# Kernel tuning notes

Hardware: AMD Instinct MI355X
Metric: run time of the kernel (lower is better)

The kernel has to match this reference:

```python
import jax, jax.numpy as jnp
import numpy as np
import math

B, S, HID = 1, 2048, 1024
NH, NKV = 16, 4
HD = HID // NH          # 64
GROUPS = NH // NKV      # 4
ROPE_BASE = 10000.0


def setup_inputs() -> dict:
    key = jax.random.key(0)
    ks = jax.random.split(key, 5)
    hidden_states = jax.random.normal(ks[0], (B, S, HID), dtype=jnp.float32)
    # additive causal mask: 0 on/below diagonal, -1e9 above
    causal = jnp.triu(jnp.full((S, S), -1e9, dtype=jnp.float32), k=1)
    attention_mask = causal[None, None, :, :]
    position_ids = jnp.arange(S, dtype=jnp.int32)[None, :]
    sc = 0.02
    Wq = jax.random.normal(ks[1], (NH * HD, HID), dtype=jnp.float32) * sc
    Wk = jax.random.normal(ks[2], (NKV * HD, HID), dtype=jnp.float32) * sc
    Wv = jax.random.normal(ks[3], (NKV * HD, HID), dtype=jnp.float32) * sc
    Wo = jax.random.normal(ks[4], (HID, NH * HD), dtype=jnp.float32) * sc
    return {"hidden_states": hidden_states, "attention_mask": attention_mask,
            "position_ids": position_ids, "Wq": Wq, "Wk": Wk, "Wv": Wv, "Wo": Wo}


def _rotate_half(x):
    x1, x2 = jnp.split(x, 2, axis=-1)
    return jnp.concatenate([-x2, x1], axis=-1)


def _rope_cos_sin(position_ids, dtype):
    # LlamaRotaryEmbedding: inv_freq over even dims, emb = [freqs, freqs]
    inv_freq = 1.0 / (ROPE_BASE ** (jnp.arange(0, HD, 2, dtype=jnp.float32) / HD))
    freqs = position_ids.astype(jnp.float32)[..., None] * inv_freq  # [B,S,HD/2]
    emb = jnp.concatenate([freqs, freqs], axis=-1)                  # [B,S,HD]
    return jnp.cos(emb).astype(dtype)[:, None], jnp.sin(emb).astype(dtype)[:, None]


def reference(hidden_states, attention_mask, position_ids, Wq, Wk, Wv, Wo):
    b, q_len, _ = hidden_states.shape
    # torch Linear: y = x @ W.T  (W is [out, in])
    q = jnp.einsum('bsh,oh->bso', hidden_states, Wq).reshape(b, q_len, NH, HD).transpose(0, 2, 1, 3)
    k = jnp.einsum('bsh,oh->bso', hidden_states, Wk).reshape(b, q_len, NKV, HD).transpose(0, 2, 1, 3)
    v = jnp.einsum('bsh,oh->bso', hidden_states, Wv).reshape(b, q_len, NKV, HD).transpose(0, 2, 1, 3)

    cos, sin = _rope_cos_sin(position_ids, q.dtype)  # [B,1,S,HD]
    q = q * cos + _rotate_half(q) * sin
    k = k * cos + _rotate_half(k) * sin

    # repeat_kv (GQA expansion)
    k = jnp.repeat(k, GROUPS, axis=1)  # [B,NH,S,HD]
    v = jnp.repeat(v, GROUPS, axis=1)

    scores = jnp.einsum('bhqd,bhkd->bhqk', q, k) / math.sqrt(HD)
    scores = scores + attention_mask
    attn = jax.nn.softmax(scores.astype(jnp.float32), axis=-1).astype(q.dtype)
    out = jnp.einsum('bhqk,bhkd->bhqd', attn, v)
    out = out.transpose(0, 2, 1, 3).reshape(b, q_len, NH * HD)
    return jnp.einsum('bso,ho->bsh', out, Wo)
```

## Files before the change

kernel.cpp:

```cpp
#include <hip/hip_runtime.h>
#include <hip/hip_bf16.h>
#include <math.h>

#define S_LEN 2048
#define HIDN  1024
#define K_DIM 1024
#define NHEAD 16
#define NKVH  4
#define HD    64

typedef __bf16 bf16x8 __attribute__((ext_vector_type(8)));
typedef float  f32x4  __attribute__((ext_vector_type(4)));

static __device__ __forceinline__ unsigned short f2bf(float f) {
  union { float f; unsigned u; } v; v.f = f;
  unsigned u = v.u;
  u += 0x7fffu + ((u >> 16) & 1u);
  return (unsigned short)(u >> 16);
}

static __device__ __forceinline__ void gload_lds16(const unsigned short* g, unsigned short* l) {
  __builtin_amdgcn_global_load_lds((const __attribute__((address_space(1))) void*)g,
                                   (__attribute__((address_space(3))) void*)l, 16, 0, 0);
}

__global__ __launch_bounds__(256) void prep_kernel(const float* __restrict__ hs,
                                                   const float* __restrict__ Wq,
                                                   const float* __restrict__ Wk,
                                                   const float* __restrict__ Wv,
                                                   const float* __restrict__ Wo,
                                                   const int* __restrict__ pos,
                                                   unsigned short* __restrict__ hsb,
                                                   unsigned short* __restrict__ Wqkv,
                                                   unsigned short* __restrict__ Wob,
                                                   float2* __restrict__ cstab) {
  const int gid = blockIdx.x * 256 + threadIdx.x;
  if (gid < 1179648) {
    const float* src; unsigned short* dst; int i;
    if (gid < 524288)       { src = hs; dst = hsb;            i = gid; }
    else if (gid < 786432)  { src = Wq; dst = Wqkv;           i = gid - 524288; }
    else if (gid < 851968)  { src = Wk; dst = Wqkv + 1048576; i = gid - 786432; }
    else if (gid < 917504)  { src = Wv; dst = Wqkv + 1310720; i = gid - 851968; }
    else                    { src = Wo; dst = Wob;            i = gid - 917504; }
    float4 v = *(const float4*)(src + (size_t)i * 4);
    ushort4 u;
    u.x = f2bf(v.x); u.y = f2bf(v.y); u.z = f2bf(v.z); u.w = f2bf(v.w);
    *(ushort4*)(dst + (size_t)i * 4) = u;
  } else {
    int e = gid - 1179648;
    int s = e >> 5, ir = e & 31;
    float p = (float)pos[s];
    float ang = p * __expf(-(float)ir * 0.28782314f);
    float c, sn;
    sincosf(ang, &sn, &c);
    cstab[e] = make_float2(c, sn);
  }
}

template <bool ROPE>
__global__ __launch_bounds__(256) void gemm_kernel(const unsigned short* __restrict__ A,
                                                   const unsigned short* __restrict__ B,
                                                   float* __restrict__ C,
                                                   const float2* __restrict__ cstab,
                                                   unsigned short* __restrict__ Qr,
                                                   unsigned short* __restrict__ Kr,
                                                   unsigned short* __restrict__ Vtmp) {
  __shared__ unsigned short As[2][64][64];
  __shared__ unsigned short Bs[2][128][64];
  const int m0 = blockIdx.x * 64, n0 = blockIdx.y * 128;
  const int t = threadIdx.x, w = t >> 6, lane = t & 63;
  const int lr = lane & 15, lg = lane >> 4;
  const int m_off = (w & 1) * 32, n_off = (w >> 1) * 64;
  const int rsub = lane >> 3;
  const int cole = ((lane & 7) * 8) ^ (rsub << 3);
  f32x4 acc[2][4] = {};

#define GSTAGE(b, kt) do {                                                     \
    _Pragma("unroll")                                                          \
    for (int c = 0; c < 2; ++c) {                                              \
      int ch = w * 2 + c;                                                      \
      gload_lds16(A + (size_t)(m0 + ch * 8 + rsub) * K_DIM + (kt) * 64 + cole, \
                  &As[b][0][0] + ch * 512);                                    \
    }                                                                          \
    _Pragma("unroll")                                                          \
    for (int c = 0; c < 4; ++c) {                                              \
      int ch = w * 4 + c;                                                      \
      gload_lds16(B + (size_t)(n0 + ch * 8 + rsub) * K_DIM + (kt) * 64 + cole, \
                  &Bs[b][0][0] + ch * 512);                                    \
    }                                                                          \
  } while (0)

  int cur = 0;
  GSTAGE(0, 0);
  for (int kt = 0; kt < 16; ++kt) {
    __syncthreads();
    if (kt + 1 < 16) GSTAGE(cur ^ 1, kt + 1);
#pragma unroll
    for (int kc = 0; kc < 2; ++kc) {
      bf16x8 af[2], bfg[4];
#pragma unroll
      for (int i = 0; i < 2; ++i) {
        int row = m_off + i * 16 + lr;
        af[i] = *(const bf16x8*)((const char*)&As[cur][0][0] + row * 128 +
                                 ((kc * 64 + lg * 16) ^ ((lr & 7) << 4)));
      }
#pragma unroll
      for (int j = 0; j < 4; ++j) {
        int row = n_off + j * 16 + lr;
        bfg[j] = *(const bf16x8*)((const char*)&Bs[cur][0][0] + row * 128 +
                                  ((kc * 64 + lg * 16) ^ ((lr & 7) << 4)));
      }
#pragma unroll
      for (int i = 0; i < 2; ++i)
#pragma unroll
        for (int j = 0; j < 4; ++j)
          acc[i][j] = __builtin_amdgcn_mfma_f32_16x16x32_bf16(af[i], bfg[j], acc[i][j], 0, 0, 0);
    }
    cur ^= 1;
  }

  if constexpr (ROPE) {
    const int col64 = n0 + n_off;
    const int hh = col64 >> 6;
#pragma unroll
    for (int i = 0; i < 2; ++i) {
#pragma unroll
      for (int r = 0; r < 4; ++r) {
        int srow = m0 + m_off + i * 16 + lg * 4 + r;
        if (hh < 20) {
          unsigned short* dst = (hh < 16) ? (Qr + ((size_t)hh * S_LEN + srow) * HD)
                                          : (Kr + ((size_t)(hh - 16) * S_LEN + srow) * HD);
          float sc = (hh < 16) ? 0.125f : 1.0f;
#pragma unroll
          for (int j = 0; j < 2; ++j) {
            int d0 = j * 16 + lr;
            float2 cs = cstab[(size_t)srow * 32 + d0];
            float v0 = acc[i][j][r] * sc, v1 = acc[i][j + 2][r] * sc;
            dst[d0]      = f2bf(v0 * cs.x - v1 * cs.y);
            dst[d0 + 32] = f2bf(v1 * cs.x + v0 * cs.y);
          }
        } else {
          int vcol = col64 - 1280;
#pragma unroll
          for (int j = 0; j < 4; ++j)
            Vtmp[(size_t)srow * 256 + vcol + j * 16 + lr] = f2bf(acc[i][j][r]);
        }
      }
    }
  } else {
#pragma unroll
    for (int i = 0; i < 2; ++i)
#pragma unroll
      for (int j = 0; j < 4; ++j)
#pragma unroll
        for (int r = 0; r < 4; ++r)
          C[(size_t)(m0 + m_off + i * 16 + lg * 4 + r) * 1024 + n0 + n_off + j * 16 + lr] =
              acc[i][j][r];
  }
}

__global__ __launch_bounds__(256) void transpose_v(const unsigned short* __restrict__ Vtmp,
                                                   unsigned short* __restrict__ Vt) {
  __shared__ unsigned short tile[64][72];
  const int kh = blockIdx.x & 3, st = blockIdx.x >> 2;
  const int s0 = st * 64;
  const int t = threadIdx.x;
  const int r = t >> 3, c = (t & 7) * 8;
#pragma unroll
  for (int p = 0; p < 2; ++p) {
    int row = r + p * 32;
    uint4 v = *(const uint4*)(Vtmp + (size_t)(s0 + row) * 256 + kh * 64 + c);
    *(uint4*)&tile[row][c] = v;
  }
  __syncthreads();
#pragma unroll
  for (int p = 0; p < 2; ++p) {
    int d = r + p * 32;
    int sc = (t & 7) * 8;
    union { unsigned short s[8]; uint4 q; } u;
#pragma unroll
    for (int e = 0; e < 8; ++e) u.s[e] = tile[sc + e][d];
    *(uint4*)(Vt + ((size_t)kh * HD + d) * S_LEN + s0 + sc) = u.q;
  }
}

__global__ __launch_bounds__(256) void attn_kernel(const unsigned short* __restrict__ Qr,
                                                   const unsigned short* __restrict__ Kr,
                                                   const unsigned short* __restrict__ Vt,
                                                   unsigned short* __restrict__ Ob) {
  __shared__ unsigned short Ks[2][64][64];
  __shared__ unsigned short Vs[2][64][64];
  const int h = blockIdx.x & 15;
  const int qt = 31 - (blockIdx.x >> 4);
  const int kh = h >> 2;
  const int q0 = qt * 64;
  const int t = threadIdx.x, w = t >> 6, lane = t & 63;
  const int lr = lane & 15, lg = lane >> 4;
  const int qabs = q0 + w * 16 + lr;
  const int src0 = ((lane >> 4) & 1) * 32 + lr;
  const int src1 = src0 + 16;
  const bool hi2 = (lg & 2);

  const unsigned short* qb = Qr + ((size_t)h * S_LEN + qabs) * HD + lg * 8;
  bf16x8 qf0 = *(const bf16x8*)qb;
  bf16x8 qf1 = *(const bf16x8*)(qb + 32);

  float m_run = -1e30f, l_run = 0.f;
  f32x4 oacc[4] = {};

  const int rsub = lane >> 3;
  const int cole = ((lane & 7) * 8) ^ (rsub << 3);

#define ASTAGE(b, kt) do {                                                        \
    int k0s = (kt) * 64;                                                          \
    _Pragma("unroll")                                                             \
    for (int c = 0; c < 4; ++c) {                                                 \
      int ch = w * 4 + c;                                                         \
      int rowc = (ch & 7) * 8 + rsub;                                             \
      if (ch < 8)                                                                 \
        gload_lds16(Kr + ((size_t)kh * S_LEN + k0s + rowc) * HD + cole,           \
                    &Ks[b][0][0] + (ch & 7) * 512);                               \
      else                                                                        \
        gload_lds16(Vt + ((size_t)kh * HD + rowc) * S_LEN + k0s + cole,           \
                    &Vs[b][0][0] + (ch & 7) * 512);                               \
    }                                                                             \
  } while (0)

  int cur = 0;
  const int nkt = qt + 1;
  ASTAGE(0, 0);
  for (int kt = 0; kt < nkt; ++kt) {
    __syncthreads();
    if (kt + 1 < nkt) ASTAGE(cur ^ 1, kt + 1);
    const int k0 = kt * 64;

    f32x4 sacc[4] = {};
#pragma unroll
    for (int kc = 0; kc < 2; ++kc) {
      bf16x8 qq = kc ? qf1 : qf0;
#pragma unroll
      for (int nt = 0; nt < 4; ++nt) {
        int row = nt * 16 + lr;
        bf16x8 kf = *(const bf16x8*)((const char*)&Ks[cur][0][0] + row * 128 +
                                     ((kc * 64 + lg * 16) ^ ((lr & 7) << 4)));
        sacc[nt] = __builtin_amdgcn_mfma_f32_16x16x32_bf16(kf, qq, sacc[nt], 0, 0, 0);
      }
    }

    float p[16];
#pragma unroll
    for (int nt = 0; nt < 4; ++nt)
#pragma unroll
      for (int r = 0; r < 4; ++r) p[nt * 4 + r] = sacc[nt][r];

    if (kt == qt) {
      int lim = qabs - k0 - lg * 4;
#pragma unroll
      for (int nt = 0; nt < 4; ++nt)
#pragma unroll
        for (int r = 0; r < 4; ++r)
          if (nt * 16 + r > lim) p[nt * 4 + r] = -1e30f;
    }

    float t0 = fmaxf(fmaxf(p[0], p[1]), fmaxf(p[2], p[3]));
    float t1 = fmaxf(fmaxf(p[4], p[5]), fmaxf(p[6], p[7]));
    float t2 = fmaxf(fmaxf(p[8], p[9]), fmaxf(p[10], p[11]));
    float t3 = fmaxf(fmaxf(p[12], p[13]), fmaxf(p[14], p[15]));
    float tmax = fmaxf(fmaxf(t0, t1), fmaxf(t2, t3));
    tmax = fmaxf(tmax, __shfl_xor(tmax, 16));
    tmax = fmaxf(tmax, __shfl_xor(tmax, 32));

    if (__any(tmax > m_run + 8.0f)) {
      float mnew = fmaxf(m_run, tmax);
      float f = __expf(m_run - mnew);
      l_run *= f;
#pragma unroll
      for (int dt = 0; dt < 4; ++dt) oacc[dt] *= f;
      m_run = mnew;
    }

    float lsum = 0.f;
#pragma unroll
    for (int e = 0; e < 16; ++e) {
      p[e] = __expf(p[e] - m_run);
      lsum += p[e];
    }
    lsum += __shfl_xor(lsum, 16);
    lsum += __shfl_xor(lsum, 32);
    l_run += lsum;

    unsigned pk[4][2];
#pragma unroll
    for (int nt = 0; nt < 4; ++nt)
#pragma unroll
      for (int rr = 0; rr < 2; ++rr) {
        union { __hip_bfloat162 b; unsigned u; } cv;
        cv.b = __float22bfloat162_rn(make_float2(p[nt * 4 + 2 * rr], p[nt * 4 + 2 * rr + 1]));
        pk[nt][rr] = cv.u;
      }

#pragma unroll
    for (int kcp = 0; kcp < 2; ++kcp) {
      const int nta = kcp * 2, ntb = kcp * 2 + 1;
      unsigned a0 = __shfl(pk[nta][0], src0), b0 = __shfl(pk[ntb][0], src0);
      unsigned a1 = __shfl(pk[nta][1], src0), b1 = __shfl(pk[ntb][1], src0);
      unsigned a2 = __shfl(pk[nta][0], src1), b2 = __shfl(pk[ntb][0], src1);
      unsigned a3 = __shfl(pk[nta][1], src1), b3 = __shfl(pk[ntb][1], src1);
      union { bf16x8 v; unsigned u[4]; } pf;
      pf.u[0] = hi2 ? b0 : a0;
      pf.u[1] = hi2 ? b1 : a1;
      pf.u[2] = hi2 ? b2 : a2;
      pf.u[3] = hi2 ? b3 : a3;
#pragma unroll
      for (int dt = 0; dt < 4; ++dt) {
        int row = dt * 16 + lr;
        bf16x8 vf = *(const bf16x8*)((const char*)&Vs[cur][0][0] + row * 128 +
                                     ((kcp * 64 + lg * 16) ^ ((lr & 7) << 4)));
        oacc[dt] = __builtin_amdgcn_mfma_f32_16x16x32_bf16(vf, pf.v, oacc[dt], 0, 0, 0);
      }
    }
    cur ^= 1;
  }

  float inv = 1.f / l_run;
#pragma unroll
  for (int dt = 0; dt < 4; ++dt) {
    ushort4 u;
    u.x = f2bf(oacc[dt][0] * inv);
    u.y = f2bf(oacc[dt][1] * inv);
    u.z = f2bf(oacc[dt][2] * inv);
    u.w = f2bf(oacc[dt][3] * inv);
    *(ushort4*)(Ob + (size_t)qabs * HIDN + h * HD + dt * 16 + lg * 4) = u;
  }
}

extern "C" void kernel_launch(void* const* d_in, const int* in_sizes, int n_in,
                              void* d_out, int out_size, void* d_ws, size_t ws_size,
                              hipStream_t stream) {
  const float* hs = (const float*)d_in[0];
  const int* pos = (const int*)d_in[2];
  const float* Wq = (const float*)d_in[3];
  const float* Wk = (const float*)d_in[4];
  const float* Wv = (const float*)d_in[5];
  const float* Wo = (const float*)d_in[6];
  float* out = (float*)d_out;

  char* ws = (char*)d_ws;
  unsigned short* hsb  = (unsigned short*)(ws);
  unsigned short* Wqkv = (unsigned short*)(ws + 4194304);
  unsigned short* Wob  = (unsigned short*)(ws + 7340032);
  float2*         cstab = (float2*)(ws + 9437184);
  unsigned short* Qr   = (unsigned short*)(ws + 10485760);
  unsigned short* Kr   = (unsigned short*)(ws + 14680064);
  unsigned short* Vtmp = (unsigned short*)(ws + 15728640);
  unsigned short* Vt   = (unsigned short*)(ws + 16777216);
  unsigned short* Ob   = (unsigned short*)(ws + 17825792);

  dim3 blk(256);
  prep_kernel<<<4864, blk, 0, stream>>>(hs, Wq, Wk, Wv, Wo, pos, hsb, Wqkv, Wob, cstab);
  gemm_kernel<true><<<dim3(32, 12), blk, 0, stream>>>(hsb, Wqkv, nullptr, cstab, Qr, Kr, Vtmp);
  transpose_v<<<128, blk, 0, stream>>>(Vtmp, Vt);
  attn_kernel<<<512, blk, 0, stream>>>(Qr, Kr, Vt, Ob);
  gemm_kernel<false><<<dim3(32, 8), blk, 0, stream>>>(Ob, Wob, out, nullptr, nullptr, nullptr, nullptr);
}
```

Measured before the change: 89.13 us.

## Split causal attention along the key dimension with a separate merge kernel

Replaces the single attention kernel with a split-KV scheme. Each query tile's key range is cut into chunks of up to 8 key tiles, which gives 1280 balanced blocks instead of 512 blocks of very uneven causal length. Each block writes fp32 partial outputs and its (max, sum) stats to workspace. A new merge kernel then rescales and combines the partials and writes the bf16 output. The cost is an extra launch and roughly 30+ MB of extra fp32 partial-output traffic.

After: 90.68 us. About the same (+1.7%).

```diff
diff --git a/kernel.cpp b/kernel.cpp
--- a/kernel.cpp
+++ b/kernel.cpp
@@ -184,16 +184,26 @@
   }
 }
 
-__global__ __launch_bounds__(256) void attn_kernel(const unsigned short* __restrict__ Qr,
-                                                   const unsigned short* __restrict__ Kr,
-                                                   const unsigned short* __restrict__ Vt,
-                                                   unsigned short* __restrict__ Ob) {
+__global__ __launch_bounds__(256) void attn_part(const unsigned short* __restrict__ Qr,
+                                                 const unsigned short* __restrict__ Kr,
+                                                 const unsigned short* __restrict__ Vt,
+                                                 float* __restrict__ Opart,
+                                                 float* __restrict__ Mlpart) {
   __shared__ unsigned short Ks[2][64][64];
   __shared__ unsigned short Vs[2][64][64];
-  const int h = blockIdx.x & 15;
-  const int qt = 31 - (blockIdx.x >> 4);
+  const int bid = blockIdx.x;
+  const int h = bid / 80;
+  const int remr = 79 - (bid - h * 80);
+  int qt, ck;
+  if (remr < 8)       { qt = remr;                 ck = 0; }
+  else if (remr < 24) { int e = remr - 8;  qt = 8  + (e >> 1); ck = e & 1; }
+  else if (remr < 48) { int e = remr - 24; int d3 = e / 3; qt = 16 + d3; ck = e - d3 * 3; }
+  else                { int e = remr - 48; qt = 24 + (e >> 2); ck = e & 3; }
   const int kh = h >> 2;
   const int q0 = qt * 64;
+  const int kt0 = ck * 8;
+  const int kt1 = (kt0 + 8 < qt + 1) ? kt0 + 8 : qt + 1;
+
   const int t = threadIdx.x, w = t >> 6, lane = t & 63;
   const int lr = lane & 15, lg = lane >> 4;
   const int qabs = q0 + w * 16 + lr;
@@ -227,11 +237,10 @@
   } while (0)
 
   int cur = 0;
-  const int nkt = qt + 1;
-  ASTAGE(0, 0);
-  for (int kt = 0; kt < nkt; ++kt) {
+  ASTAGE(0, kt0);
+  for (int kt = kt0; kt < kt1; ++kt) {
     __syncthreads();
-    if (kt + 1 < nkt) ASTAGE(cur ^ 1, kt + 1);
+    if (kt + 1 < kt1) ASTAGE(cur ^ 1, kt + 1);
     const int k0 = kt * 64;
 
     f32x4 sacc[4] = {};
@@ -322,15 +331,54 @@
     cur ^= 1;
   }
 
-  float inv = 1.f / l_run;
+  const int slot = (h * 32 + qt) * 4 + ck;
+  float* ob = Opart + (size_t)slot * 4096;
+#pragma unroll
+  for (int dt = 0; dt < 4; ++dt)
+    *(f32x4*)(ob + (((w * 4 + dt) * 4 + lg) * 16 + lr) * 4) = oacc[dt];
+  if (lg == 0)
+    *(float2*)(Mlpart + ((size_t)slot * 64 + w * 16 + lr) * 2) = make_float2(m_run, l_run);
+}
+
+__global__ __launch_bounds__(256) void attn_merge(const float* __restrict__ Opart,
+                                                  const float* __restrict__ Mlpart,
+                                                  unsigned short* __restrict__ Ob) {
+  const int h = blockIdx.x >> 5, qt = blockIdx.x & 31;
+  const int nch = (qt >> 3) + 1;
+  const int slotb = (h * 32 + qt) * 4;
+  const int t = threadIdx.x, w = t >> 6, lane = t & 63;
+  const int lr = lane & 15, lg = lane >> 4;
+  const int q = w * 16 + lr;
+
+  float mc[4], lc[4];
+  float mstar = -1e30f;
+  for (int c = 0; c < nch; ++c) {
+    float2 ml = *(const float2*)(Mlpart + ((size_t)(slotb + c) * 64 + q) * 2);
+    mc[c] = ml.x; lc[c] = ml.y;
+    mstar = fmaxf(mstar, ml.x);
+  }
+  float wgt[4];
+  float lsum = 0.f;
+  for (int c = 0; c < nch; ++c) {
+    wgt[c] = __expf(mc[c] - mstar);
+    lsum += wgt[c] * lc[c];
+  }
+  const float inv = 1.f / lsum;
+
 #pragma unroll
   for (int dt = 0; dt < 4; ++dt) {
+    f32x4 a = {};
+    for (int c = 0; c < nch; ++c) {
+      f32x4 v = *(const f32x4*)(Opart + (size_t)(slotb + c) * 4096 +
+                                (((w * 4 + dt) * 4 + lg) * 16 + lr) * 4);
+      a += v * wgt[c];
+    }
     ushort4 u;
-    u.x = f2bf(oacc[dt][0] * inv);
-    u.y = f2bf(oacc[dt][1] * inv);
-    u.z = f2bf(oacc[dt][2] * inv);
-    u.w = f2bf(oacc[dt][3] * inv);
-    *(ushort4*)(Ob + (size_t)qabs * HIDN + h * HD + dt * 16 + lg * 4) = u;
+    u.x = f2bf(a[0] * inv);
+    u.y = f2bf(a[1] * inv);
+    u.z = f2bf(a[2] * inv);
+    u.w = f2bf(a[3] * inv);
+    *(ushort4*)(Ob + (size_t)(qt * 64 + q) * HIDN + h * HD + dt * 16 + lg * 4) = u;
   }
 }
 
@@ -346,20 +394,23 @@
   float* out = (float*)d_out;
 
   char* ws = (char*)d_ws;
-  unsigned short* hsb  = (unsigned short*)(ws);
-  unsigned short* Wqkv = (unsigned short*)(ws + 4194304);
-  unsigned short* Wob  = (unsigned short*)(ws + 7340032);
+  unsigned short* hsb   = (unsigned short*)(ws);
+  unsigned short* Wqkv  = (unsigned short*)(ws + 4194304);
+  unsigned short* Wob   = (unsigned short*)(ws + 7340032);
   float2*         cstab = (float2*)(ws + 9437184);
-  unsigned short* Qr   = (unsigned short*)(ws + 10485760);
-  unsigned short* Kr   = (unsigned short*)(ws + 14680064);
-  unsigned short* Vtmp = (unsigned short*)(ws + 15728640);
-  unsigned short* Vt   = (unsigned short*)(ws + 16777216);
-  unsigned short* Ob   = (unsigned short*)(ws + 17825792);
+  unsigned short* Qr    = (unsigned short*)(ws + 10485760);
+  unsigned short* Kr    = (unsigned short*)(ws + 14680064);
+  unsigned short* Vtmp  = (unsigned short*)(ws + 15728640);
+  unsigned short* Vt    = (unsigned short*)(ws + 16777216);
+  unsigned short* Ob    = (unsigned short*)(ws + 17825792);
+  float*          Opart = (float*)(ws + 22020096);
+  float*          Mlpart= (float*)(ws + 55574528);
 
   dim3 blk(256);
   prep_kernel<<<4864, blk, 0, stream>>>(hs, Wq, Wk, Wv, Wo, pos, hsb, Wqkv, Wob, cstab);
   gemm_kernel<true><<<dim3(32, 12), blk, 0, stream>>>(hsb, Wqkv, nullptr, cstab, Qr, Kr, Vtmp);
   transpose_v<<<128, blk, 0, stream>>>(Vtmp, Vt);
-  attn_kernel<<<512, blk, 0, stream>>>(Qr, Kr, Vt, Ob);
+  attn_part<<<1280, blk, 0, stream>>>(Qr, Kr, Vt, Opart, Mlpart);
+  attn_merge<<<512, blk, 0, stream>>>(Opart, Mlpart, Ob);
   gemm_kernel<false><<<dim3(32, 8), blk, 0, stream>>>(Ob, Wob, out, nullptr, nullptr, nullptr, nullptr);
 }
```

## Replace LDS-staged attention block with single-wave blocks reading K/V directly

Applied to the files above, without the earlier changes.

Attention now runs as 2048 one-wave blocks, each handling a 16-query strip, instead of 512 four-wave blocks per 64-query tile. The LDS double-buffering and __syncthreads are removed, and K and V fragments are loaded straight from global memory (through cache), with V prefetched into registers before the softmax. s_setprio is added around the MFMA sections. This finer split aims to improve load balance across the causal triangle and remove sync overhead, at the cost of losing K/V reuse across the four waves that previously shared each LDS tile, which raises global/L2 traffic.

Measured after the change: 119.6 us. 34.2% more time.

```diff
diff --git a/kernel.cpp b/kernel.cpp
--- a/kernel.cpp
+++ b/kernel.cpp
@@ -184,19 +184,18 @@
   }
 }
 
-__global__ __launch_bounds__(256) void attn_kernel(const unsigned short* __restrict__ Qr,
-                                                   const unsigned short* __restrict__ Kr,
-                                                   const unsigned short* __restrict__ Vt,
-                                                   unsigned short* __restrict__ Ob) {
-  __shared__ unsigned short Ks[2][64][64];
-  __shared__ unsigned short Vs[2][64][64];
-  const int h = blockIdx.x & 15;
-  const int qt = 31 - (blockIdx.x >> 4);
+__global__ __launch_bounds__(64) void attn_wave(const unsigned short* __restrict__ Qr,
+                                                const unsigned short* __restrict__ Kr,
+                                                const unsigned short* __restrict__ Vt,
+                                                unsigned short* __restrict__ Ob) {
+  const int bid = blockIdx.x;
+  const int h = bid & 15;
+  const int strip = 127 - (bid >> 4);
   const int kh = h >> 2;
-  const int q0 = qt * 64;
-  const int t = threadIdx.x, w = t >> 6, lane = t & 63;
+  const int q0 = strip * 16;
+  const int lane = threadIdx.x;
   const int lr = lane & 15, lg = lane >> 4;
-  const int qabs = q0 + w * 16 + lr;
+  const int qabs = q0 + lr;
   const int src0 = ((lane >> 4) & 1) * 32 + lr;
   const int src1 = src0 + 16;
   const bool hi2 = (lg & 2);
@@ -205,47 +204,35 @@
   bf16x8 qf0 = *(const bf16x8*)qb;
   bf16x8 qf1 = *(const bf16x8*)(qb + 32);
 
+  const unsigned short* Kh = Kr + (size_t)kh * S_LEN * HD;
+  const unsigned short* Vh = Vt + (size_t)kh * HD * S_LEN;
+
   float m_run = -1e30f, l_run = 0.f;
   f32x4 oacc[4] = {};
-
-  const int rsub = lane >> 3;
-  const int cole = ((lane & 7) * 8) ^ (rsub << 3);
-
-#define ASTAGE(b, kt) do {                                                        \
-    int k0s = (kt) * 64;                                                          \
-    _Pragma("unroll")                                                             \
-    for (int c = 0; c < 4; ++c) {                                                 \
-      int ch = w * 4 + c;                                                         \
-      int rowc = (ch & 7) * 8 + rsub;                                             \
-      if (ch < 8)                                                                 \
-        gload_lds16(Kr + ((size_t)kh * S_LEN + k0s + rowc) * HD + cole,           \
-                    &Ks[b][0][0] + (ch & 7) * 512);                               \
-      else                                                                        \
-        gload_lds16(Vt + ((size_t)kh * HD + rowc) * S_LEN + k0s + cole,           \
-                    &Vs[b][0][0] + (ch & 7) * 512);                               \
-    }                                                                             \
-  } while (0)
-
-  int cur = 0;
-  const int nkt = qt + 1;
-  ASTAGE(0, 0);
+  const int nkt = (q0 >> 6) + 1;
+
   for (int kt = 0; kt < nkt; ++kt) {
-    __syncthreads();
-    if (kt + 1 < nkt) ASTAGE(cur ^ 1, kt + 1);
     const int k0 = kt * 64;
 
     f32x4 sacc[4] = {};
+    __builtin_amdgcn_s_setprio(1);
 #pragma unroll
     for (int kc = 0; kc < 2; ++kc) {
       bf16x8 qq = kc ? qf1 : qf0;
 #pragma unroll
       for (int nt = 0; nt < 4; ++nt) {
-        int row = nt * 16 + lr;
-        bf16x8 kf = *(const bf16x8*)((const char*)&Ks[cur][0][0] + row * 128 +
-                                     ((kc * 64 + lg * 16) ^ ((lr & 7) << 4)));
+        bf16x8 kf = *(const bf16x8*)(Kh + (size_t)(k0 + nt * 16 + lr) * HD + kc * 32 + lg * 8);
         sacc[nt] = __builtin_amdgcn_mfma_f32_16x16x32_bf16(kf, qq, sacc[nt], 0, 0, 0);
       }
     }
+    __builtin_amdgcn_s_setprio(0);
+
+    bf16x8 vf[2][4];
+#pragma unroll
+    for (int kcp = 0; kcp < 2; ++kcp)
+#pragma unroll
+      for (int dt = 0; dt < 4; ++dt)
+        vf[kcp][dt] = *(const bf16x8*)(Vh + (size_t)(dt * 16 + lr) * S_LEN + k0 + kcp * 32 + lg * 8);
 
     float p[16];
 #pragma unroll
@@ -253,7 +240,7 @@
 #pragma unroll
       for (int r = 0; r < 4; ++r) p[nt * 4 + r] = sacc[nt][r];
 
-    if (kt == qt) {
+    if (kt == nkt - 1) {
       int lim = qabs - k0 - lg * 4;
 #pragma unroll
       for (int nt = 0; nt < 4; ++nt)
@@ -311,15 +298,12 @@
       pf.u[1] = hi2 ? b1 : a1;
       pf.u[2] = hi2 ? b2 : a2;
       pf.u[3] = hi2 ? b3 : a3;
-#pragma unroll
-      for (int dt = 0; dt < 4; ++dt) {
-        int row = dt * 16 + lr;
-        bf16x8 vf = *(const bf16x8*)((const char*)&Vs[cur][0][0] + row * 128 +
-                                     ((kcp * 64 + lg * 16) ^ ((lr & 7) << 4)));
-        oacc[dt] = __builtin_amdgcn_mfma_f32_16x16x32_bf16(vf, pf.v, oacc[dt], 0, 0, 0);
-      }
-    }
-    cur ^= 1;
+      __builtin_amdgcn_s_setprio(1);
+#pragma unroll
+      for (int dt = 0; dt < 4; ++dt)
+        oacc[dt] = __builtin_amdgcn_mfma_f32_16x16x32_bf16(vf[kcp][dt], pf.v, oacc[dt], 0, 0, 0);
+      __builtin_amdgcn_s_setprio(0);
+    }
   }
 
   float inv = 1.f / l_run;
@@ -346,20 +330,20 @@
   float* out = (float*)d_out;
 
   char* ws = (char*)d_ws;
-  unsigned short* hsb  = (unsigned short*)(ws);
-  unsigned short* Wqkv = (unsigned short*)(ws + 4194304);
-  unsigned short* Wob  = (unsigned short*)(ws + 7340032);
+  unsigned short* hsb   = (unsigned short*)(ws);
+  unsigned short* Wqkv  = (unsigned short*)(ws + 4194304);
+  unsigned short* Wob   = (unsigned short*)(ws + 7340032);
   float2*         cstab = (float2*)(ws + 9437184);
-  unsigned short* Qr   = (unsigned short*)(ws + 10485760);
-  unsigned short* Kr   = (unsigned short*)(ws + 14680064);
-  unsigned short* Vtmp = (unsigned short*)(ws + 15728640);
-  unsigned short* Vt   = (unsigned short*)(ws + 16777216);
-  unsigned short* Ob   = (unsigned short*)(ws + 17825792);
+  unsigned short* Qr    = (unsigned short*)(ws + 10485760);
+  unsigned short* Kr    = (unsigned short*)(ws + 14680064);
+  unsigned short* Vtmp  = (unsigned short*)(ws + 15728640);
+  unsigned short* Vt    = (unsigned short*)(ws + 16777216);
+  unsigned short* Ob    = (unsigned short*)(ws + 17825792);
 
   dim3 blk(256);
   prep_kernel<<<4864, blk, 0, stream>>>(hs, Wq, Wk, Wv, Wo, pos, hsb, Wqkv, Wob, cstab);
   gemm_kernel<true><<<dim3(32, 12), blk, 0, stream>>>(hsb, Wqkv, nullptr, cstab, Qr, Kr, Vtmp);
   transpose_v<<<128, blk, 0, stream>>>(Vtmp, Vt);
-  attn_kernel<<<512, blk, 0, stream>>>(Qr, Kr, Vt, Ob);
+  attn_wave<<<2048, dim3(64), 0, stream>>>(Qr, Kr, Vt, Ob);
   gemm_kernel<false><<<dim3(32, 8), blk, 0, stream>>>(Ob, Wob, out, nullptr, nullptr, nullptr, nullptr);
 }
```
